# Kernel optimization log

Hardware: AMD Instinct MI355X
Metric: run time of the kernel (lower is better)

The kernel has to match this reference:

```python
import jax, jax.numpy as jnp
import numpy as np

S = 1024          # num tokens (single prefill sequence)
H = 2880          # hidden_size
NH = 64           # num query heads
NKV = 8           # num kv heads
HD = 64           # head_dim
G = NH // NKV     # query heads per kv head
THETA = 10000.0
SCALE = HD ** -0.5


def _rope(x, positions):
    # neox-style rotary over full head_dim; x: [S, n_heads, HD]
    half = HD // 2
    inv_freq = 1.0 / (THETA ** (jnp.arange(half, dtype=jnp.float32) / half))
    ang = positions.astype(jnp.float32)[:, None] * inv_freq          # [S, half]
    cos = jnp.cos(ang)[:, None, :]
    sin = jnp.sin(ang)[:, None, :]
    x1, x2 = x[..., :half], x[..., half:]
    return jnp.concatenate([x1 * cos - x2 * sin, x2 * cos + x1 * sin], axis=-1)


def setup_inputs() -> dict:
    key = jax.random.key(0)
    k0, k1, k2, k3 = jax.random.split(key, 4)
    return {
        "positions": jnp.arange(S, dtype=jnp.int32),
        "hidden_states": jax.random.normal(k0, (S, H), dtype=jnp.float32),
        "qkv_w": jax.random.normal(k1, ((NH + 2 * NKV) * HD, H), dtype=jnp.float32) * 0.02,
        "o_w": jax.random.normal(k2, (H, NH * HD), dtype=jnp.float32) * 0.02,
        "sinks": jax.random.normal(k3, (NH,), dtype=jnp.float32),
    }


def reference(positions, hidden_states, qkv_w, o_w, sinks):
    # fused QKV projection (no bias, matching attention_bias=False)
    qkv = hidden_states @ qkv_w.T                                     # [S, 5120]
    q = qkv[:, : NH * HD].reshape(S, NH, HD)
    k = qkv[:, NH * HD : NH * HD + NKV * HD].reshape(S, NKV, HD)
    v = qkv[:, NH * HD + NKV * HD :].reshape(S, NKV, HD)

    # rotary on q and k (rotary_dim == head_dim)
    q = _rope(q, positions)
    k = _rope(k, positions)

    # GQA: group query heads by kv head -> [S, NKV, G, HD]
    qg = q.reshape(S, NKV, G, HD)

    logits = jnp.einsum("qghd,kgd->ghqk", qg, k) * SCALE              # [NKV, G, S, S]
    causal = positions[:, None] >= positions[None, :]                 # [S, S]
    logits = jnp.where(causal[None, None], logits, -jnp.inf)

    # attention sinks: per-head extra logit in the softmax denominator,
    # contributing no value vector.
    sink = sinks.reshape(NKV, G)[:, :, None, None]                    # [NKV, G, 1, 1]
    m = jnp.maximum(jnp.max(logits, axis=-1, keepdims=True), sink)
    p = jnp.exp(logits - m)                                           # [NKV, G, S, S]
    denom = jnp.sum(p, axis=-1, keepdims=True) + jnp.exp(sink - m)
    attn = jnp.einsum("ghqk,kgd->qghd", p / denom, v)                 # [S, NKV, G, HD]

    out = attn.reshape(S, NH * HD) @ o_w.T                            # [S, H]
    return out
```

## Files before the change

### kernel.cpp

```cpp
#include <hip/hip_runtime.h>
#include <hip/hip_bf16.h>
#include <math.h>

#define S_LEN 1024
#define HDIM  2880
#define NH    64
#define NKV   8
#define HD    64
#define QKV_N ((NH + 2*NKV) * HD)
#define O_K   (NH * HD)
#define SCALE 0.125f

typedef _Float16 f16x8 __attribute__((ext_vector_type(8)));
typedef _Float16 f16x4 __attribute__((ext_vector_type(4)));
typedef float    f32x4 __attribute__((ext_vector_type(4)));

__global__ __launch_bounds__(256) void cvt3_f32_f16(
    const float* __restrict__ a, _Float16* __restrict__ da, int na4,
    const float* __restrict__ b, _Float16* __restrict__ db, int nb4,
    const float* __restrict__ c, _Float16* __restrict__ dc, int nc4) {
    const int stride = gridDim.x * blockDim.x;
    const int tot = na4 + nb4 + nc4;
    for (int i = blockIdx.x * blockDim.x + threadIdx.x; i < tot; i += stride) {
        const float* s; _Float16* d; int j = i;
        if (j < na4)            { s = a; d = da; }
        else if (j < na4 + nb4) { j -= na4; s = b; d = db; }
        else                    { j -= na4 + nb4; s = c; d = dc; }
        const float4 v = ((const float4*)s)[j];
        f16x4 p;
        p[0] = (_Float16)v.x; p[1] = (_Float16)v.y;
        p[2] = (_Float16)v.z; p[3] = (_Float16)v.w;
        ((f16x4*)d)[j] = p;
    }
}

template<bool B_F32, typename CT>
__global__ __launch_bounds__(256) void gemm_f16(const _Float16* __restrict__ A,
                                                const void* __restrict__ Bp,
                                                CT* __restrict__ C,
                                                int M, int N, int K) {
    __shared__ __align__(16) _Float16 As[128 * 32];
    __shared__ __align__(16) _Float16 Bs[128 * 32];

    const int tid  = threadIdx.x;
    const int lane = tid & 63;
    const int wave = tid >> 6;
    const int wr   = wave >> 1;
    const int wc   = wave & 1;
    const int row0 = blockIdx.y * 128;
    const int col0 = blockIdx.x * 128;

    const int klen = K / (int)gridDim.z;
    const int kb   = (int)blockIdx.z * klen;
    CT* Cp = C + (size_t)blockIdx.z * M * N;

    const int fr = lane & 15;
    const int ks = (lane >> 4) * 8;

    f32x4 acc[4][4] = {};

    for (int k0 = kb; k0 < kb + klen; k0 += 32) {
        __syncthreads();
#pragma unroll
        for (int it = 0; it < 2; ++it) {
            const int cbase = it * 256 + wave * 64;
            const int ci = cbase + lane;
            const int r  = ci >> 2;
            const int ch = ci & 3;
            const _Float16* gp = A + (size_t)(row0 + r) * K + k0 + ch * 8;
            __builtin_amdgcn_global_load_lds(
                (const __attribute__((address_space(1))) void*)gp,
                (__attribute__((address_space(3))) void*)(As + (size_t)cbase * 8),
                16, 0, 0);
        }
        if constexpr (B_F32) {
            const float* B = (const float*)Bp;
#pragma unroll
            for (int it = 0; it < 4; ++it) {
                const int c4 = it * 256 + tid;
                const int r  = c4 >> 3;
                const int ch = (c4 & 7) << 2;
                int brow = col0 + r;
                if (brow >= N) brow = N - 1;
                const float4 bv = *(const float4*)&B[(size_t)brow * K + k0 + ch];
                f16x4 p;
                p[0] = (_Float16)bv.x; p[1] = (_Float16)bv.y;
                p[2] = (_Float16)bv.z; p[3] = (_Float16)bv.w;
                *(f16x4*)&Bs[r * 32 + ch] = p;
            }
        } else {
            const _Float16* B = (const _Float16*)Bp;
#pragma unroll
            for (int it = 0; it < 2; ++it) {
                const int cbase = it * 256 + wave * 64;
                const int ci = cbase + lane;
                const int r  = ci >> 2;
                const int ch = ci & 3;
                int brow = col0 + r;
                if (brow >= N) brow = N - 1;
                const _Float16* gp = B + (size_t)brow * K + k0 + ch * 8;
                __builtin_amdgcn_global_load_lds(
                    (const __attribute__((address_space(1))) void*)gp,
                    (__attribute__((address_space(3))) void*)(Bs + (size_t)cbase * 8),
                    16, 0, 0);
            }
        }
        __syncthreads();

        f16x8 af[4], bfr[4];
#pragma unroll
        for (int mi = 0; mi < 4; ++mi)
            af[mi] = *(const f16x8*)&As[(wr * 64 + mi * 16 + fr) * 32 + ks];
#pragma unroll
        for (int ni = 0; ni < 4; ++ni)
            bfr[ni] = *(const f16x8*)&Bs[(wc * 64 + ni * 16 + fr) * 32 + ks];
#pragma unroll
        for (int mi = 0; mi < 4; ++mi)
#pragma unroll
            for (int ni = 0; ni < 4; ++ni)
                acc[mi][ni] = __builtin_amdgcn_mfma_f32_16x16x32_f16(
                    af[mi], bfr[ni], acc[mi][ni], 0, 0, 0);
    }

#pragma unroll
    for (int ni = 0; ni < 4; ++ni) {
        const int col = col0 + wc * 64 + ni * 16 + fr;
        if (col >= N) continue;
#pragma unroll
        for (int mi = 0; mi < 4; ++mi) {
            const int rbase = row0 + wr * 64 + mi * 16 + (lane >> 4) * 4;
            const f32x4 v = acc[mi][ni];
            Cp[(size_t)(rbase + 0) * N + col] = (CT)v[0];
            Cp[(size_t)(rbase + 1) * N + col] = (CT)v[1];
            Cp[(size_t)(rbase + 2) * N + col] = (CT)v[2];
            Cp[(size_t)(rbase + 3) * N + col] = (CT)v[3];
        }
    }
}

__global__ __launch_bounds__(256) void rope_reduce(_Float16* __restrict__ parts,
                                                   int nsplit,
                                                   _Float16* __restrict__ vt,
                                                   const int* __restrict__ positions) {
    __shared__ float buf[QKV_N];
    const int s   = blockIdx.x;
    const int tid = threadIdx.x;
    const size_t PSTR = (size_t)S_LEN * QKV_N;

    for (int c = tid; c < QKV_N / 4; c += 256) {
        float4 a = make_float4(0.f, 0.f, 0.f, 0.f);
        for (int j = 0; j < nsplit; ++j) {
            const f16x4 v = ((const f16x4*)(parts + j * PSTR + (size_t)s * QKV_N))[c];
            a.x += (float)v[0]; a.y += (float)v[1];
            a.z += (float)v[2]; a.w += (float)v[3];
        }
        ((float4*)buf)[c] = a;
    }
    __syncthreads();

    const float pos = (float)positions[s];
    _Float16* orow = parts + (size_t)s * QKV_N;
    for (int w = tid; w < 72 * 32; w += 256) {
        const int h = w >> 5;
        const int t = w & 31;
        const float inv_freq = exp2f(-(float)t * (13.287712379549449f / 32.0f));
        const float ang = pos * inv_freq;
        float sn, cs;
        sincosf(ang, &sn, &cs);
        const float x1 = buf[h * 64 + t];
        const float x2 = buf[h * 64 + t + 32];
        orow[h * 64 + t]      = (_Float16)(x1 * cs - x2 * sn);
        orow[h * 64 + t + 32] = (_Float16)(x2 * cs + x1 * sn);
    }
    for (int c = tid; c < NKV * HD; c += 256)
        vt[(size_t)c * S_LEN + s] = (_Float16)buf[(NH + NKV) * HD + c];
}

__global__ __launch_bounds__(256) void o_reduce(const _Float16* __restrict__ parts,
                                                float* __restrict__ out,
                                                int n4, int nsplit) {
    const size_t PSTR = (size_t)S_LEN * HDIM;
    const int stride = gridDim.x * blockDim.x;
    for (int i = blockIdx.x * blockDim.x + threadIdx.x; i < n4; i += stride) {
        float4 a = make_float4(0.f, 0.f, 0.f, 0.f);
        for (int j = 0; j < nsplit; ++j) {
            const f16x4 v = ((const f16x4*)(parts + j * PSTR))[i];
            a.x += (float)v[0]; a.y += (float)v[1];
            a.z += (float)v[2]; a.w += (float)v[3];
        }
        ((float4*)out)[i] = a;
    }
}

#define LSTR 72
__global__ __launch_bounds__(256) void attn_mfma(const _Float16* __restrict__ qkv,
                                                 const _Float16* __restrict__ vt,
                                                 const float* __restrict__ sinks,
                                                 const int* __restrict__ positions,
                                                 _Float16* __restrict__ attn_out) {
    __shared__ __align__(16) _Float16 Ks[64 * LSTR];
    __shared__ __align__(16) _Float16 Vs[64 * LSTR];
    __shared__ __align__(16) _Float16 Ps[64 * LSTR];
    __shared__ int posk[64];

    const int tid  = threadIdx.x;
    const int lane = tid & 63;
    const int wave = tid >> 6;
    const int fr   = lane & 15;
    const int quad = lane >> 4;
    const int ks8  = quad * 8;
    const int n    = blockIdx.x;
    const int qt   = (int)gridDim.y - 1 - (int)blockIdx.y;
    const int g    = n >> 3;

    const _Float16* qrow = qkv + (size_t)(qt * 64 + wave * 16 + fr) * QKV_N + n * HD;
    const f16x8 a_q0 = *(const f16x8*)&qrow[ks8];
    const f16x8 a_q1 = *(const f16x8*)&qrow[32 + ks8];

    int pq[4];
#pragma unroll
    for (int r = 0; r < 4; ++r)
        pq[r] = positions[qt * 64 + wave * 16 + quad * 4 + r];

    const float sinkv = sinks[n];
    float m[4], l[4];
    f32x4 o[4] = {};
#pragma unroll
    for (int r = 0; r < 4; ++r) { m[r] = sinkv; l[r] = 1.0f; }

    for (int kt = 0; kt <= qt; ++kt) {
        __syncthreads();
        const _Float16* Kg = qkv + (size_t)(kt * 64) * QKV_N + NH * HD + g * HD;
        const _Float16* Vg = vt + (size_t)(g * HD) * S_LEN + kt * 64;
#pragma unroll
        for (int it = 0; it < 2; ++it) {
            const int c = it * 256 + tid;
            const int r = c >> 3, off8 = (c & 7) * 8;
            const f16x8 kv = *(const f16x8*)&Kg[(size_t)r * QKV_N + off8];
            *(f16x8*)&Ks[r * LSTR + off8] = kv;
            const f16x8 vv = *(const f16x8*)&Vg[(size_t)r * S_LEN + off8];
            *(f16x8*)&Vs[r * LSTR + off8] = vv;
        }
        if (tid < 64) posk[tid] = positions[kt * 64 + tid];
        __syncthreads();

        f32x4 s[4] = {};
#pragma unroll
        for (int nt = 0; nt < 4; ++nt) {
            const f16x8 b0 = *(const f16x8*)&Ks[(nt * 16 + fr) * LSTR + ks8];
            s[nt] = __builtin_amdgcn_mfma_f32_16x16x32_f16(a_q0, b0, s[nt], 0, 0, 0);
            const f16x8 b1 = *(const f16x8*)&Ks[(nt * 16 + fr) * LSTR + 32 + ks8];
            s[nt] = __builtin_amdgcn_mfma_f32_16x16x32_f16(a_q1, b1, s[nt], 0, 0, 0);
        }

        const bool diag = (kt == qt);
        int pk[4];
        if (diag) {
#pragma unroll
            for (int nt = 0; nt < 4; ++nt) pk[nt] = posk[nt * 16 + fr];
        }
#pragma unroll
        for (int nt = 0; nt < 4; ++nt)
#pragma unroll
            for (int r = 0; r < 4; ++r) {
                float sv = s[nt][r] * SCALE;
                if (diag && pk[nt] > pq[r]) sv = -3.0e38f;
                s[nt][r] = sv;
            }

#pragma unroll
        for (int r = 0; r < 4; ++r) {
            float tm = fmaxf(fmaxf(s[0][r], s[1][r]), fmaxf(s[2][r], s[3][r]));
            tm = fmaxf(tm, __shfl_xor(tm, 1, 64));
            tm = fmaxf(tm, __shfl_xor(tm, 2, 64));
            tm = fmaxf(tm, __shfl_xor(tm, 4, 64));
            tm = fmaxf(tm, __shfl_xor(tm, 8, 64));
            const float nm = fmaxf(m[r], tm);
            const float alpha = __expf(m[r] - nm);
            float rs = 0.0f;
#pragma unroll
            for (int nt = 0; nt < 4; ++nt) {
                const float p = __expf(s[nt][r] - nm);
                s[nt][r] = p;
                rs += p;
            }
            rs += __shfl_xor(rs, 1, 64);
            rs += __shfl_xor(rs, 2, 64);
            rs += __shfl_xor(rs, 4, 64);
            rs += __shfl_xor(rs, 8, 64);
            l[r] = l[r] * alpha + rs;
            m[r] = nm;
#pragma unroll
            for (int nt = 0; nt < 4; ++nt) o[nt][r] *= alpha;
        }

#pragma unroll
        for (int nt = 0; nt < 4; ++nt)
#pragma unroll
            for (int r = 0; r < 4; ++r)
                Ps[(wave * 16 + quad * 4 + r) * LSTR + nt * 16 + fr] = (_Float16)s[nt][r];
        __threadfence_block();

#pragma unroll
        for (int k2 = 0; k2 < 2; ++k2) {
            const f16x8 ap = *(const f16x8*)&Ps[(wave * 16 + fr) * LSTR + k2 * 32 + ks8];
#pragma unroll
            for (int nt = 0; nt < 4; ++nt) {
                const f16x8 bv = *(const f16x8*)&Vs[(nt * 16 + fr) * LSTR + k2 * 32 + ks8];
                o[nt] = __builtin_amdgcn_mfma_f32_16x16x32_f16(ap, bv, o[nt], 0, 0, 0);
            }
        }
    }

#pragma unroll
    for (int r = 0; r < 4; ++r) {
        const float inv = 1.0f / l[r];
        const size_t row = (size_t)(qt * 64 + wave * 16 + quad * 4 + r);
#pragma unroll
        for (int nt = 0; nt < 4; ++nt)
            attn_out[row * O_K + n * HD + nt * 16 + fr] = (_Float16)(o[nt][r] * inv);
    }
}

extern "C" void kernel_launch(void* const* d_in, const int* in_sizes, int n_in,
                              void* d_out, int out_size, void* d_ws, size_t ws_size,
                              hipStream_t stream) {
    const int*   positions = (const int*)d_in[0];
    const float* hidden    = (const float*)d_in[1];
    const float* qkv_w     = (const float*)d_in[2];
    const float* o_w       = (const float*)d_in[3];
    const float* sinks     = (const float*)d_in[4];
    float* out = (float*)d_out;

    const size_t n_qkvw = (size_t)QKV_N * HDIM;
    const size_t n_ow   = (size_t)HDIM * O_K;
    const size_t n_hid  = (size_t)S_LEN * HDIM;
    const size_t n_qkv  = (size_t)S_LEN * QKV_N;
    const size_t n_attn = (size_t)S_LEN * O_K;
    const size_t n_vt   = (size_t)NKV * HD * S_LEN;
    const size_t n_out  = (size_t)S_LEN * HDIM;

    const int SP_Q = 3;
    const int SP_O = 4;

    const size_t need1 = (n_qkvw + n_ow + n_hid + SP_Q * n_qkv + n_attn + n_vt) * 2;
    const size_t need2 = (n_hid + SP_Q * n_qkv + n_attn + n_vt + SP_O * n_out) * 2;

    if (ws_size >= need1) {
        _Float16* qkv_w_h = (_Float16*)d_ws;
        _Float16* o_w_h   = qkv_w_h + n_qkvw;
        _Float16* hid_h   = o_w_h + n_ow;
        _Float16* qkvp    = hid_h + n_hid;
        _Float16* attn_h  = qkvp + SP_Q * n_qkv;
        _Float16* vt      = attn_h + n_attn;
        _Float16* opart   = qkv_w_h;

        cvt3_f32_f16<<<2048, 256, 0, stream>>>(hidden, hid_h, (int)(n_hid / 4),
                                               qkv_w, qkv_w_h, (int)(n_qkvw / 4),
                                               o_w, o_w_h, (int)(n_ow / 4));
        gemm_f16<false, _Float16><<<dim3(QKV_N / 128, S_LEN / 128, SP_Q), 256, 0, stream>>>(
            hid_h, qkv_w_h, qkvp, S_LEN, QKV_N, HDIM);
        rope_reduce<<<S_LEN, 256, 0, stream>>>(qkvp, SP_Q, vt, positions);
        attn_mfma<<<dim3(NH, S_LEN / 64), 256, 0, stream>>>(qkvp, vt, sinks, positions, attn_h);
        gemm_f16<false, _Float16><<<dim3((HDIM + 127) / 128, S_LEN / 128, SP_O), 256, 0, stream>>>(
            attn_h, o_w_h, opart, S_LEN, HDIM, O_K);
        o_reduce<<<1024, 256, 0, stream>>>(opart, out, (int)(n_out / 4), SP_O);
    } else if (ws_size >= need2) {
        _Float16* hid_h  = (_Float16*)d_ws;
        _Float16* qkvp   = hid_h + n_hid;
        _Float16* attn_h = qkvp + SP_Q * n_qkv;
        _Float16* vt     = attn_h + n_attn;
        _Float16* opart  = vt + n_vt;

        cvt3_f32_f16<<<1024, 256, 0, stream>>>(hidden, hid_h, (int)(n_hid / 4),
                                               nullptr, nullptr, 0, nullptr, nullptr, 0);
        gemm_f16<true, _Float16><<<dim3(QKV_N / 128, S_LEN / 128, SP_Q), 256, 0, stream>>>(
            hid_h, qkv_w, qkvp, S_LEN, QKV_N, HDIM);
        rope_reduce<<<S_LEN, 256, 0, stream>>>(qkvp, SP_Q, vt, positions);
        attn_mfma<<<dim3(NH, S_LEN / 64), 256, 0, stream>>>(qkvp, vt, sinks, positions, attn_h);
        gemm_f16<true, _Float16><<<dim3((HDIM + 127) / 128, S_LEN / 128, SP_O), 256, 0, stream>>>(
            attn_h, o_w, opart, S_LEN, HDIM, O_K);
        o_reduce<<<1024, 256, 0, stream>>>(opart, out, (int)(n_out / 4), SP_O);
    } else {
        _Float16* hid_h  = (_Float16*)d_ws;
        _Float16* qkvp   = hid_h + n_hid;
        _Float16* attn_h = qkvp + n_qkv;
        _Float16* vt     = attn_h + n_attn;

        cvt3_f32_f16<<<1024, 256, 0, stream>>>(hidden, hid_h, (int)(n_hid / 4),
                                               nullptr, nullptr, 0, nullptr, nullptr, 0);
        gemm_f16<true, _Float16><<<dim3(QKV_N / 128, S_LEN / 128, 1), 256, 0, stream>>>(
            hid_h, qkv_w, qkvp, S_LEN, QKV_N, HDIM);
        rope_reduce<<<S_LEN, 256, 0, stream>>>(qkvp, 1, vt, positions);
        attn_mfma<<<dim3(NH, S_LEN / 64), 256, 0, stream>>>(qkvp, vt, sinks, positions, attn_h);
        gemm_f16<true, float><<<dim3((HDIM + 127) / 128, S_LEN / 128, 1), 256, 0, stream>>>(
            attn_h, o_w, out, S_LEN, HDIM, O_K);
    }
}
```

Before: 305.8 us.

## Convert weights in GEMM loaders, stage epilogue through LDS, raise split-K

Drops the separate f32-to-f16 pre-conversion pass for both weight matrices. The GEMMs now always read f32 weights and convert them while staging into shared memory, so the extra weight read-write round trip through workspace is gone. The GEMM epilogue is rewritten to stage accumulators in padded shared memory and write 8-wide vectorized rows instead of scattered scalar column stores. Split-K factors rise from 3/4 to 6/8, which adds grid parallelism but means more partial buffers to reduce. The trade-off is twice the global weight bytes per tile and a synchronous conversion in the load loop.

```diff
diff --git a/kernel.cpp b/kernel.cpp
--- a/kernel.cpp
+++ b/kernel.cpp
@@ -15,47 +15,42 @@
 typedef _Float16 f16x4 __attribute__((ext_vector_type(4)));
 typedef float    f32x4 __attribute__((ext_vector_type(4)));
 
-__global__ __launch_bounds__(256) void cvt3_f32_f16(
-    const float* __restrict__ a, _Float16* __restrict__ da, int na4,
-    const float* __restrict__ b, _Float16* __restrict__ db, int nb4,
-    const float* __restrict__ c, _Float16* __restrict__ dc, int nc4) {
+__global__ __launch_bounds__(256) void cvt_f32_f16(const float* __restrict__ src,
+                                                   _Float16* __restrict__ dst, int n4) {
     const int stride = gridDim.x * blockDim.x;
-    const int tot = na4 + nb4 + nc4;
-    for (int i = blockIdx.x * blockDim.x + threadIdx.x; i < tot; i += stride) {
-        const float* s; _Float16* d; int j = i;
-        if (j < na4)            { s = a; d = da; }
-        else if (j < na4 + nb4) { j -= na4; s = b; d = db; }
-        else                    { j -= na4 + nb4; s = c; d = dc; }
-        const float4 v = ((const float4*)s)[j];
+    for (int i = blockIdx.x * blockDim.x + threadIdx.x; i < n4; i += stride) {
+        const float4 v = ((const float4*)src)[i];
         f16x4 p;
         p[0] = (_Float16)v.x; p[1] = (_Float16)v.y;
         p[2] = (_Float16)v.z; p[3] = (_Float16)v.w;
-        ((f16x4*)d)[j] = p;
-    }
-}
-
-template<bool B_F32, typename CT>
+        ((f16x4*)dst)[i] = p;
+    }
+}
+
+#define CSTR 68
+template<typename CT>
 __global__ __launch_bounds__(256) void gemm_f16(const _Float16* __restrict__ A,
-                                                const void* __restrict__ Bp,
+                                                const float* __restrict__ B,
                                                 CT* __restrict__ C,
                                                 int M, int N, int K) {
-    __shared__ __align__(16) _Float16 As[128 * 32];
-    __shared__ __align__(16) _Float16 Bs[128 * 32];
+    __shared__ __align__(16) _Float16 sh[128 * CSTR];
+    _Float16* As = sh;
+    _Float16* Bs = sh + 4096;
 
     const int tid  = threadIdx.x;
     const int lane = tid & 63;
     const int wave = tid >> 6;
     const int wr   = wave >> 1;
     const int wc   = wave & 1;
+    const int quad = lane >> 4;
+    const int fr   = lane & 15;
+    const int ks   = quad * 8;
     const int row0 = blockIdx.y * 128;
     const int col0 = blockIdx.x * 128;
 
     const int klen = K / (int)gridDim.z;
     const int kb   = (int)blockIdx.z * klen;
     CT* Cp = C + (size_t)blockIdx.z * M * N;
-
-    const int fr = lane & 15;
-    const int ks = (lane >> 4) * 8;
 
     f32x4 acc[4][4] = {};
 
@@ -73,37 +68,18 @@
                 (__attribute__((address_space(3))) void*)(As + (size_t)cbase * 8),
                 16, 0, 0);
         }
-        if constexpr (B_F32) {
-            const float* B = (const float*)Bp;
-#pragma unroll
-            for (int it = 0; it < 4; ++it) {
-                const int c4 = it * 256 + tid;
-                const int r  = c4 >> 3;
-                const int ch = (c4 & 7) << 2;
-                int brow = col0 + r;
-                if (brow >= N) brow = N - 1;
-                const float4 bv = *(const float4*)&B[(size_t)brow * K + k0 + ch];
-                f16x4 p;
-                p[0] = (_Float16)bv.x; p[1] = (_Float16)bv.y;
-                p[2] = (_Float16)bv.z; p[3] = (_Float16)bv.w;
-                *(f16x4*)&Bs[r * 32 + ch] = p;
-            }
-        } else {
-            const _Float16* B = (const _Float16*)Bp;
-#pragma unroll
-            for (int it = 0; it < 2; ++it) {
-                const int cbase = it * 256 + wave * 64;
-                const int ci = cbase + lane;
-                const int r  = ci >> 2;
-                const int ch = ci & 3;
-                int brow = col0 + r;
-                if (brow >= N) brow = N - 1;
-                const _Float16* gp = B + (size_t)brow * K + k0 + ch * 8;
-                __builtin_amdgcn_global_load_lds(
-                    (const __attribute__((address_space(1))) void*)gp,
-                    (__attribute__((address_space(3))) void*)(Bs + (size_t)cbase * 8),
-                    16, 0, 0);
-            }
+#pragma unroll
+        for (int it = 0; it < 4; ++it) {
+            const int c4 = it * 256 + tid;
+            const int r  = c4 >> 3;
+            const int ch = (c4 & 7) << 2;
+            int brow = col0 + r;
+            if (brow >= N) brow = N - 1;
+            const float4 bv = *(const float4*)&B[(size_t)brow * K + k0 + ch];
+            f16x4 p;
+            p[0] = (_Float16)bv.x; p[1] = (_Float16)bv.y;
+            p[2] = (_Float16)bv.z; p[3] = (_Float16)bv.w;
+            *(f16x4*)&Bs[r * 32 + ch] = p;
         }
         __syncthreads();
 
@@ -123,17 +99,44 @@
     }
 
 #pragma unroll
-    for (int ni = 0; ni < 4; ++ni) {
-        const int col = col0 + wc * 64 + ni * 16 + fr;
-        if (col >= N) continue;
-#pragma unroll
-        for (int mi = 0; mi < 4; ++mi) {
-            const int rbase = row0 + wr * 64 + mi * 16 + (lane >> 4) * 4;
-            const f32x4 v = acc[mi][ni];
-            Cp[(size_t)(rbase + 0) * N + col] = (CT)v[0];
-            Cp[(size_t)(rbase + 1) * N + col] = (CT)v[1];
-            Cp[(size_t)(rbase + 2) * N + col] = (CT)v[2];
-            Cp[(size_t)(rbase + 3) * N + col] = (CT)v[3];
+    for (int p = 0; p < 2; ++p) {
+        __syncthreads();
+        if (wc == p) {
+#pragma unroll
+            for (int mi = 0; mi < 4; ++mi)
+#pragma unroll
+                for (int ni = 0; ni < 4; ++ni) {
+                    const f32x4 v = acc[mi][ni];
+#pragma unroll
+                    for (int r = 0; r < 4; ++r)
+                        sh[(wr * 64 + mi * 16 + quad * 4 + r) * CSTR + ni * 16 + fr] =
+                            (_Float16)v[r];
+                }
+        }
+        __syncthreads();
+#pragma unroll
+        for (int it = 0; it < 4; ++it) {
+            const int id  = it * 256 + tid;
+            const int row = id >> 3;
+            const int ch  = (id & 7) * 8;
+            const int col = col0 + p * 64 + ch;
+            if (col < N) {
+                const f16x4 lo = *(const f16x4*)&sh[row * CSTR + ch];
+                const f16x4 hi = *(const f16x4*)&sh[row * CSTR + ch + 4];
+                if constexpr (sizeof(CT) == 2) {
+                    f16x8 v;
+                    v[0]=lo[0]; v[1]=lo[1]; v[2]=lo[2]; v[3]=lo[3];
+                    v[4]=hi[0]; v[5]=hi[1]; v[6]=hi[2]; v[7]=hi[3];
+                    *(f16x8*)&Cp[(size_t)(row0 + row) * N + col] = v;
+                } else {
+                    float4 v0 = make_float4((float)lo[0], (float)lo[1],
+                                            (float)lo[2], (float)lo[3]);
+                    float4 v1 = make_float4((float)hi[0], (float)hi[1],
+                                            (float)hi[2], (float)hi[3]);
+                    *(float4*)&Cp[(size_t)(row0 + row) * N + col]     = v0;
+                    *(float4*)&Cp[(size_t)(row0 + row) * N + col + 4] = v1;
+                }
+            }
         }
     }
 }
@@ -332,53 +335,30 @@
     const float* sinks     = (const float*)d_in[4];
     float* out = (float*)d_out;
 
-    const size_t n_qkvw = (size_t)QKV_N * HDIM;
-    const size_t n_ow   = (size_t)HDIM * O_K;
     const size_t n_hid  = (size_t)S_LEN * HDIM;
     const size_t n_qkv  = (size_t)S_LEN * QKV_N;
     const size_t n_attn = (size_t)S_LEN * O_K;
     const size_t n_vt   = (size_t)NKV * HD * S_LEN;
     const size_t n_out  = (size_t)S_LEN * HDIM;
 
-    const int SP_Q = 3;
-    const int SP_O = 4;
-
-    const size_t need1 = (n_qkvw + n_ow + n_hid + SP_Q * n_qkv + n_attn + n_vt) * 2;
-    const size_t need2 = (n_hid + SP_Q * n_qkv + n_attn + n_vt + SP_O * n_out) * 2;
-
-    if (ws_size >= need1) {
-        _Float16* qkv_w_h = (_Float16*)d_ws;
-        _Float16* o_w_h   = qkv_w_h + n_qkvw;
-        _Float16* hid_h   = o_w_h + n_ow;
-        _Float16* qkvp    = hid_h + n_hid;
-        _Float16* attn_h  = qkvp + SP_Q * n_qkv;
-        _Float16* vt      = attn_h + n_attn;
-        _Float16* opart   = qkv_w_h;
-
-        cvt3_f32_f16<<<2048, 256, 0, stream>>>(hidden, hid_h, (int)(n_hid / 4),
-                                               qkv_w, qkv_w_h, (int)(n_qkvw / 4),
-                                               o_w, o_w_h, (int)(n_ow / 4));
-        gemm_f16<false, _Float16><<<dim3(QKV_N / 128, S_LEN / 128, SP_Q), 256, 0, stream>>>(
-            hid_h, qkv_w_h, qkvp, S_LEN, QKV_N, HDIM);
-        rope_reduce<<<S_LEN, 256, 0, stream>>>(qkvp, SP_Q, vt, positions);
-        attn_mfma<<<dim3(NH, S_LEN / 64), 256, 0, stream>>>(qkvp, vt, sinks, positions, attn_h);
-        gemm_f16<false, _Float16><<<dim3((HDIM + 127) / 128, S_LEN / 128, SP_O), 256, 0, stream>>>(
-            attn_h, o_w_h, opart, S_LEN, HDIM, O_K);
-        o_reduce<<<1024, 256, 0, stream>>>(opart, out, (int)(n_out / 4), SP_O);
-    } else if (ws_size >= need2) {
+    const int SP_Q = 6;
+    const int SP_O = 8;
+
+    const size_t need = (n_hid + SP_Q * n_qkv + n_attn + n_vt) * sizeof(_Float16);
+
+    if (ws_size >= need) {
         _Float16* hid_h  = (_Float16*)d_ws;
         _Float16* qkvp   = hid_h + n_hid;
         _Float16* attn_h = qkvp + SP_Q * n_qkv;
         _Float16* vt     = attn_h + n_attn;
-        _Float16* opart  = vt + n_vt;
-
-        cvt3_f32_f16<<<1024, 256, 0, stream>>>(hidden, hid_h, (int)(n_hid / 4),
-                                               nullptr, nullptr, 0, nullptr, nullptr, 0);
-        gemm_f16<true, _Float16><<<dim3(QKV_N / 128, S_LEN / 128, SP_Q), 256, 0, stream>>>(
+        _Float16* opart  = qkvp;
+
+        cvt_f32_f16<<<512, 256, 0, stream>>>(hidden, hid_h, (int)(n_hid / 4));
+        gemm_f16<_Float16><<<dim3(QKV_N / 128, S_LEN / 128, SP_Q), 256, 0, stream>>>(
             hid_h, qkv_w, qkvp, S_LEN, QKV_N, HDIM);
         rope_reduce<<<S_LEN, 256, 0, stream>>>(qkvp, SP_Q, vt, positions);
         attn_mfma<<<dim3(NH, S_LEN / 64), 256, 0, stream>>>(qkvp, vt, sinks, positions, attn_h);
-        gemm_f16<true, _Float16><<<dim3((HDIM + 127) / 128, S_LEN / 128, SP_O), 256, 0, stream>>>(
+        gemm_f16<_Float16><<<dim3((HDIM + 127) / 128, S_LEN / 128, SP_O), 256, 0, stream>>>(
             attn_h, o_w, opart, S_LEN, HDIM, O_K);
         o_reduce<<<1024, 256, 0, stream>>>(opart, out, (int)(n_out / 4), SP_O);
     } else {
@@ -387,13 +367,12 @@
         _Float16* attn_h = qkvp + n_qkv;
         _Float16* vt     = attn_h + n_attn;
 
-        cvt3_f32_f16<<<1024, 256, 0, stream>>>(hidden, hid_h, (int)(n_hid / 4),
-                                               nullptr, nullptr, 0, nullptr, nullptr, 0);
-        gemm_f16<true, _Float16><<<dim3(QKV_N / 128, S_LEN / 128, 1), 256, 0, stream>>>(
+        cvt_f32_f16<<<512, 256, 0, stream>>>(hidden, hid_h, (int)(n_hid / 4));
+        gemm_f16<_Float16><<<dim3(QKV_N / 128, S_LEN / 128, 1), 256, 0, stream>>>(
             hid_h, qkv_w, qkvp, S_LEN, QKV_N, HDIM);
         rope_reduce<<<S_LEN, 256, 0, stream>>>(qkvp, 1, vt, positions);
         attn_mfma<<<dim3(NH, S_LEN / 64), 256, 0, stream>>>(qkvp, vt, sinks, positions, attn_h);
-        gemm_f16<true, float><<<dim3((HDIM + 127) / 128, S_LEN / 128, 1), 256, 0, stream>>>(
+        gemm_f16<float><<<dim3((HDIM + 127) / 128, S_LEN / 128, 1), 256, 0, stream>>>(
             attn_h, o_w, out, S_LEN, HDIM, O_K);
     }
 }
```

Measured after the change: 331.0 us. 8.2% more time.
